# Kernel tuning notes

Hardware: AMD Instinct MI355X
Metric: run time of the kernel (lower is better)

The kernel has to match this reference:

```python
import jax, jax.numpy as jnp
import numpy as np

B, S, E = 2, 2048, 1024
H = 16
DH = E // H
FF = 4096
LN_EPS = 1e-5


def setup_inputs() -> dict:
    key = jax.random.key(0)
    ks = jax.random.split(key, 8)
    s_in = 1.0 / np.sqrt(E)
    s_ff = 1.0 / np.sqrt(FF)
    return {
        "x": jax.random.normal(ks[0], (B, S, E), dtype=jnp.float32),
        "w_qkv": jax.random.normal(ks[1], (E, 3 * E), dtype=jnp.float32) * s_in,
        "b_qkv": jnp.zeros((3 * E,), dtype=jnp.float32),
        "w_proj": jax.random.normal(ks[2], (E, E), dtype=jnp.float32) * s_in,
        "b_proj": jnp.zeros((E,), dtype=jnp.float32),
        "ln_g": jnp.ones((E,), dtype=jnp.float32),
        "ln_b": jnp.zeros((E,), dtype=jnp.float32),
        "w1": jax.random.normal(ks[3], (E, FF), dtype=jnp.float32) * s_in,
        "b1": jnp.zeros((FF,), dtype=jnp.float32),
        "w2": jax.random.normal(ks[4], (FF, E), dtype=jnp.float32) * s_ff,
        "b2": jnp.zeros((E,), dtype=jnp.float32),
    }


def reference(x, w_qkv, b_qkv, w_proj, b_proj, ln_g, ln_b, w1, b1, w2, b2):
    b, s, e = x.shape
    scale = e ** 0.5  # NOTE: original scales by sqrt(embed_dim), not sqrt(head_dim)
    # qkv projection then raw view to [B,3,H,S,Dh] (faithful to torch .view)
    qkv = (x @ w_qkv + b_qkv).reshape(b, 3, H, s, DH)
    q, k, v = qkv[:, 0], qkv[:, 1], qkv[:, 2]  # each [B,H,S,Dh]
    scores = jnp.einsum("bhqd,bhkd->bhqk", q, k) / scale  # [B,H,S,S]
    causal = jnp.tril(jnp.ones((s, s), dtype=bool))
    scores = jnp.where(causal, scores, -jnp.inf)
    attn = jax.nn.softmax(scores, axis=-1)
    h = jnp.einsum("bhqk,bhkd->bhqd", attn, v)  # [B,H,S,Dh]
    h = h.reshape(b, s, e)  # faithful raw view back to [B,S,E]
    h = h @ w_proj + b_proj  # dropout = identity (eval)
    # add & norm
    h = h + x
    mu = jnp.mean(h, axis=-1, keepdims=True)
    var = jnp.var(h, axis=-1, keepdims=True)
    h = (h - mu) * jax.lax.rsqrt(var + LN_EPS) * ln_g + ln_b
    # FFN (dropouts = identity in eval)
    out = jax.nn.relu(h @ w1 + b1) @ w2 + b2
    return out
```

## Files before the change

### kernel.cpp

```cpp
#include <hip/hip_runtime.h>

#define B_ 2
#define S_ 2048
#define E_ 1024
#define H_ 16
#define DH_ 64
#define FF_ 4096

typedef unsigned short bf16_t;
typedef __attribute__((ext_vector_type(8))) short bfrag;
typedef __attribute__((ext_vector_type(4))) float f32x4;
typedef __attribute__((ext_vector_type(16))) float f32x16;
typedef __attribute__((ext_vector_type(4))) unsigned int u32x4;

__device__ __forceinline__ bf16_t f2bf(float x) {
  union { float f; unsigned u; } c; c.f = x;
  return (bf16_t)((c.u + 0x7fffu + ((c.u >> 16) & 1u)) >> 16);
}

__device__ __forceinline__ unsigned pkbf(float lo, float hi) {
  unsigned r;
  asm("v_cvt_pk_bf16_f32 %0, %1, %2" : "=v"(r) : "v"(lo), "v"(hi));
  return r;
}

__device__ __forceinline__ void gload16(const void* g, void* l) {
  __builtin_amdgcn_global_load_lds(
      (const __attribute__((address_space(1))) void*)g,
      (__attribute__((address_space(3))) void*)l, 16, 0, 0);
}

__global__ __launch_bounds__(256) void cvt_kernel(const float* __restrict__ s,
                                                  bf16_t* __restrict__ d) {
  const int i = blockIdx.x * 256 + threadIdx.x;
  const float4 v = ((const float4*)s)[i];
  union { bf16_t u[4]; uint2 uv; } o;
  o.u[0] = f2bf(v.x); o.u[1] = f2bf(v.y); o.u[2] = f2bf(v.z); o.u[3] = f2bf(v.w);
  *(uint2*)(d + (size_t)i * 4) = o.uv;
}

__global__ void transpose_cvt(const float* __restrict__ src, bf16_t* __restrict__ dst,
                              int R, int C) {
  __shared__ float tile[32][33];
  const int c0 = blockIdx.x * 32, r0 = blockIdx.y * 32;
  const int tx = threadIdx.x, ty = threadIdx.y;
#pragma unroll
  for (int i = 0; i < 32; i += 8)
    tile[ty + i][tx] = src[(size_t)(r0 + ty + i) * C + c0 + tx];
  __syncthreads();
#pragma unroll
  for (int i = 0; i < 32; i += 8)
    dst[(size_t)(c0 + ty + i) * R + r0 + tx] = f2bf(tile[tx][ty + i]);
}

__global__ void vtrans_kernel(const bf16_t* __restrict__ qkv, bf16_t* __restrict__ vt) {
  const int bh = blockIdx.z;
  const int b = bh >> 4, h = bh & 15;
  const bf16_t* src = qkv + (size_t)b * S_ * 3 * E_ + (size_t)2 * H_ * S_ * DH_ +
                      (size_t)h * S_ * DH_;
  bf16_t* dst = vt + (size_t)bh * DH_ * S_;
  const int s0 = blockIdx.x * 32, d0 = blockIdx.y * 32;
  __shared__ bf16_t tile[32][33];
  const int tx = threadIdx.x, ty = threadIdx.y;
#pragma unroll
  for (int i = 0; i < 32; i += 8)
    tile[ty + i][tx] = src[(size_t)(s0 + ty + i) * DH_ + d0 + tx];
  __syncthreads();
#pragma unroll
  for (int i = 0; i < 32; i += 8)
    dst[(size_t)(d0 + ty + i) * S_ + s0 + tx] = tile[tx][ty + i];
}


__device__ __forceinline__ void stage_half(const bf16_t* __restrict__ G, int row0,
                                           int kbyte, int Kbytes, bf16_t* ldsreg,
                                           int w, int l) {
#pragma unroll
  for (int j = 0; j < 2; ++j) {
    const int chunk = j * 8 + w;
    const int r = chunk * 8 + (l >> 3);
    const int slot = ((l & 7) ^ (r & 7)) << 4;
    const char* src = (const char*)G + (size_t)(row0 + r) * Kbytes + kbyte + slot;
    gload16(src, (char*)ldsreg + chunk * 1024);
  }
}

__device__ __forceinline__ bfrag ldfrag(const bf16_t* __restrict__ reg, int r, int ks,
                                        int l) {
  int cb = ks * 64 + ((l >> 4) << 4);
  cb ^= (r & 7) << 4;
  return *(const bfrag*)((const char*)reg + r * 128 + cb);
}

template <int MODE>
__global__ __launch_bounds__(512, 2) void gemm8(
    const bf16_t* __restrict__ A, const bf16_t* __restrict__ Bt,
    const float* __restrict__ bias, const float* __restrict__ resid,
    float* __restrict__ outF, bf16_t* __restrict__ outB,
    int M, int N, int K, int ktiles) {
  __shared__ __align__(16) bf16_t lds4[4][256 * 64];
  const int tid = threadIdx.x;
  const int w = tid >> 6, l = tid & 63;
  const int wr = (w >> 2) * 128, wc = (w & 3) * 64;
  const int m0t = blockIdx.y * 256, n0t = blockIdx.x * 256;
  const int Kb = K * 2;
  const int kt0 = (MODE == 4) ? (int)blockIdx.z * ktiles : 0;
  const int ktEnd = kt0 + ktiles;
  if (MODE == 4) outF += (size_t)blockIdx.z * (size_t)M * N;

  stage_half(A, m0t, kt0 * 128, Kb, lds4[0], w, l);
  stage_half(A, m0t + 128, kt0 * 128, Kb, lds4[0] + 8192, w, l);
  stage_half(Bt, n0t, kt0 * 128, Kb, lds4[1], w, l);
  stage_half(Bt, n0t + 128, kt0 * 128, Kb, lds4[1] + 8192, w, l);
  stage_half(Bt, n0t, (kt0 + 1) * 128, Kb, lds4[3], w, l);
  stage_half(Bt, n0t + 128, (kt0 + 1) * 128, Kb, lds4[3] + 8192, w, l);
  asm volatile("s_waitcnt vmcnt(4)" ::: "memory");
  __builtin_amdgcn_s_barrier();

  f32x4 acc[8][4] = {};
  const int fr = l & 15;

  for (int t2 = kt0; t2 < ktEnd; t2 += 2) {
#pragma unroll
    for (int d = 0; d < 2; ++d) {
      const bf16_t* Ar = lds4[d * 2];
      const bf16_t* Br = lds4[d * 2 + 1];
      int sa = t2 + 1 + d; if (sa >= ktEnd) sa = kt0;
      int sb = t2 + 2 + d; if (sb >= ktEnd) sb = kt0;
      bfrag bfr[4][2], afr[2][2];
#pragma unroll
      for (int p = 0; p < 4; ++p) {
        if (p == 0) {
#pragma unroll
          for (int n = 0; n < 4; ++n)
#pragma unroll
            for (int ks = 0; ks < 2; ++ks)
              bfr[n][ks] = ldfrag(Br, wc + n * 16 + fr, ks, l);
        }
#pragma unroll
        for (int mm = 0; mm < 2; ++mm)
#pragma unroll
          for (int ks = 0; ks < 2; ++ks)
            afr[mm][ks] = ldfrag(Ar, wr + p * 32 + mm * 16 + fr, ks, l);
        if (p == 0)      stage_half(A, m0t, sa * 128, Kb, lds4[(d ^ 1) * 2], w, l);
        else if (p == 1) stage_half(A, m0t + 128, sa * 128, Kb, lds4[(d ^ 1) * 2] + 8192, w, l);
        else if (p == 2) stage_half(Bt, n0t, sb * 128, Kb, lds4[d * 2 + 1], w, l);
        else             stage_half(Bt, n0t + 128, sb * 128, Kb, lds4[d * 2 + 1] + 8192, w, l);
        __builtin_amdgcn_s_barrier();
        asm volatile("s_waitcnt lgkmcnt(0)" ::: "memory");
        __builtin_amdgcn_sched_barrier(0);
        __builtin_amdgcn_s_setprio(1);
#pragma unroll
        for (int mm = 0; mm < 2; ++mm)
#pragma unroll
          for (int n = 0; n < 4; ++n)
#pragma unroll
            for (int ks = 0; ks < 2; ++ks)
              acc[p * 2 + mm][n] = __builtin_amdgcn_mfma_f32_16x16x32_bf16(
                  afr[mm][ks], bfr[n][ks], acc[p * 2 + mm][n], 0, 0, 0);
        __builtin_amdgcn_s_setprio(0);
        if (p == 3) asm volatile("s_waitcnt vmcnt(4)" ::: "memory");
        __builtin_amdgcn_s_barrier();
      }
    }
  }

  const int cr = (l >> 4) * 4, cc = l & 15;
#pragma unroll
  for (int n = 0; n < 4; ++n) {
    const int gc = n0t + wc + n * 16 + cc;
    const float bn = (MODE == 4) ? 0.f : bias[gc];
#pragma unroll
    for (int m = 0; m < 8; ++m) {
      const int gr0 = m0t + wr + m * 16 + cr;
#pragma unroll
      for (int j = 0; j < 4; ++j) {
        float v = acc[m][n][j] + bn;
        const size_t idx = (size_t)(gr0 + j) * N + gc;
        if (MODE == 1) v += resid[idx];
        if (MODE == 2) v = fmaxf(v, 0.f);
        if (MODE == 0 || MODE == 2) outB[idx] = f2bf(v);
        else outF[idx] = v;
      }
    }
  }
}

__global__ __launch_bounds__(256) void red4_kernel(const float* __restrict__ p,
                                                   const float* __restrict__ bias,
                                                   float* __restrict__ out) {
  const size_t i = ((size_t)blockIdx.x * 256 + threadIdx.x) * 4;
  const size_t PS = (size_t)4096 * 1024;
  const float4 a = *(const float4*)(p + i);
  const float4 b = *(const float4*)(p + PS + i);
  const float4 c = *(const float4*)(p + 2 * PS + i);
  const float4 d = *(const float4*)(p + 3 * PS + i);
  const float4 bb = *(const float4*)(bias + (i & 1023));
  float4 o;
  o.x = a.x + b.x + c.x + d.x + bb.x;
  o.y = a.y + b.y + c.y + d.y + bb.y;
  o.z = a.z + b.z + c.z + d.z + bb.z;
  o.w = a.w + b.w + c.w + d.w + bb.w;
  *(float4*)(out + i) = o;
}

#define C1_ 0.0450842213f

template <bool MASK>
__device__ __forceinline__ void attn_step(const bf16_t* __restrict__ Kp,
                                          const bf16_t* __restrict__ Vt,
                                          int kv0, const bfrag* qf, f32x16& o0,
                                          f32x16& o1, float& m, float& lsum,
                                          int lq32, int hi) {
  bfrag kf[4];
#pragma unroll
  for (int c = 0; c < 4; ++c)
    kf[c] = *(const bfrag*)&Kp[(size_t)(kv0 + lq32) * DH_ + c * 16 + hi * 8];
  f32x16 st;
#pragma unroll
  for (int j = 0; j < 16; ++j) st[j] = 0.f;
#pragma unroll
  for (int c = 0; c < 4; ++c)
    st = __builtin_amdgcn_mfma_f32_32x32x16_bf16(kf[c], qf[c], st, 0, 0, 0);
  if (MASK) {
#pragma unroll
    for (int r = 0; r < 16; ++r) {
      const int kvloc = (r & 3) + 8 * (r >> 2) + 4 * hi;
      st[r] = (kvloc <= lq32) ? st[r] : -3.0e38f;
    }
  }
  float pm = st[0];
#pragma unroll
  for (int j = 1; j < 16; ++j) pm = fmaxf(pm, st[j]);
  pm = fmaxf(pm, __shfl_xor(pm, 32));
  if (!__all(pm <= m + 128.0f)) {
    const float mn = fmaxf(m, pm);
    const float corr = exp2f((m - mn) * C1_);
    m = mn;
    lsum *= corr;
#pragma unroll
    for (int j = 0; j < 16; ++j) { o0[j] *= corr; o1[j] *= corr; }
  }
  const float mc = m * C1_;
  float p[16];
  float ps = 0.f;
#pragma unroll
  for (int j = 0; j < 16; ++j) {
    p[j] = exp2f(__builtin_fmaf(st[j], C1_, -mc));
    ps += p[j];
  }
  ps += __shfl_xor(ps, 32);
  lsum += ps;
  unsigned wv[8], ov[8];
#pragma unroll
  for (int j = 0; j < 8; ++j) wv[j] = pkbf(p[2 * j], p[2 * j + 1]);
#pragma unroll
  for (int j = 0; j < 8; ++j) ov[j] = (unsigned)__shfl_xor((int)wv[j], 32);
  union { unsigned u[4]; bfrag f; } f0, f1;
  f0.u[0] = hi ? ov[2] : wv[0];
  f0.u[1] = hi ? ov[3] : wv[1];
  f0.u[2] = hi ? wv[2] : ov[0];
  f0.u[3] = hi ? wv[3] : ov[1];
  f1.u[0] = hi ? ov[6] : wv[4];
  f1.u[1] = hi ? ov[7] : wv[5];
  f1.u[2] = hi ? wv[6] : ov[4];
  f1.u[3] = hi ? wv[7] : ov[5];
#pragma unroll
  for (int t = 0; t < 2; ++t) {
    const bf16_t* vr = &Vt[(size_t)(t * 32 + lq32) * S_ + kv0 + hi * 8];
    bfrag v0 = *(const bfrag*)vr;
    bfrag v1 = *(const bfrag*)(vr + 16);
    f32x16& ot = t ? o1 : o0;
    ot = __builtin_amdgcn_mfma_f32_32x32x16_bf16(v0, f0.f, ot, 0, 0, 0);
    ot = __builtin_amdgcn_mfma_f32_32x32x16_bf16(v1, f1.f, ot, 0, 0, 0);
  }
}

__global__ __launch_bounds__(256, 3) void attn_kernel(const bf16_t* __restrict__ qkv,
                                                      const bf16_t* __restrict__ vt,
                                                      bf16_t* __restrict__ outp) {
  __shared__ unsigned short ot[4][32 * 72];
  const int tid = threadIdx.x;
  const int w = tid >> 6, l = tid & 63;
  const int lq32 = l & 31, hi = l >> 5;
  const int by = blockIdx.y;
  const int b = by >> 4, h = by & 15;
  const int qt = (by & 16) ? (15 - (int)blockIdx.x) : (int)blockIdx.x;
  const size_t bbase = (size_t)b * S_ * 3 * E_;
  const bf16_t* Q = qkv + bbase + (size_t)h * S_ * DH_;
  const bf16_t* Kp = Q + (size_t)H_ * S_ * DH_;
  const bf16_t* Vt = vt + (size_t)by * DH_ * S_;
  bf16_t* Og = outp + (size_t)by * S_ * DH_;
  const int q0w = qt * 128 + w * 32;

  bfrag qf[4];
#pragma unroll
  for (int c = 0; c < 4; ++c)
    qf[c] = *(const bfrag*)&Q[(size_t)(q0w + lq32) * DH_ + c * 16 + hi * 8];

  f32x16 o0, o1;
#pragma unroll
  for (int j = 0; j < 16; ++j) { o0[j] = 0.f; o1[j] = 0.f; }
  float m = -3.0e38f, lsum = 0.f;

  const int nfull = q0w >> 5;
  for (int s = 0; s < nfull; ++s)
    attn_step<false>(Kp, Vt, s * 32, qf, o0, o1, m, lsum, lq32, hi);
  attn_step<true>(Kp, Vt, q0w, qf, o0, o1, m, lsum, lq32, hi);

  const float linv = 1.0f / lsum;
  unsigned short* otw = ot[w];
#pragma unroll
  for (int t = 0; t < 2; ++t) {
    const f32x16& oo = t ? o1 : o0;
#pragma unroll
    for (int g = 0; g < 4; ++g) {
      const int d = t * 32 + g * 8 + hi * 4;
      uint2 v;
      v.x = pkbf(oo[g * 4 + 0] * linv, oo[g * 4 + 1] * linv);
      v.y = pkbf(oo[g * 4 + 2] * linv, oo[g * 4 + 3] * linv);
      *(uint2*)&otw[lq32 * 72 + d] = v;
    }
  }
  asm volatile("s_waitcnt lgkmcnt(0)" ::: "memory");
  const int q = l >> 1, hh = l & 1;
#pragma unroll
  for (int i = 0; i < 4; ++i) {
    u32x4 v = *(const u32x4*)&otw[q * 72 + hh * 32 + i * 8];
    *(u32x4*)&Og[(size_t)(q0w + q) * DH_ + hh * 32 + i * 8] = v;
  }
}

__global__ __launch_bounds__(256) void ln_kernel(const float* __restrict__ hin,
                                                 const float* __restrict__ g,
                                                 const float* __restrict__ be,
                                                 bf16_t* __restrict__ outp) {
  const int row = blockIdx.x;
  const int t = threadIdx.x;
  const float4 v = ((const float4*)(hin + (size_t)row * E_))[t];
  float s = v.x + v.y + v.z + v.w;
  float q = v.x * v.x + v.y * v.y + v.z * v.z + v.w * v.w;
#pragma unroll
  for (int d = 1; d < 64; d <<= 1) { s += __shfl_xor(s, d); q += __shfl_xor(q, d); }
  __shared__ float red[8];
  const int w = t >> 6;
  if ((t & 63) == 0) { red[w] = s; red[4 + w] = q; }
  __syncthreads();
  s = red[0] + red[1] + red[2] + red[3];
  q = red[4] + red[5] + red[6] + red[7];
  const float mu = s * (1.f / E_);
  const float var = q * (1.f / E_) - mu * mu;
  const float rs = rsqrtf(var + 1e-5f);
  const float4 gg = ((const float4*)g)[t];
  const float4 bb = ((const float4*)be)[t];
  union { bf16_t u[4]; uint2 uv; } o;
  o.u[0] = f2bf((v.x - mu) * rs * gg.x + bb.x);
  o.u[1] = f2bf((v.y - mu) * rs * gg.y + bb.y);
  o.u[2] = f2bf((v.z - mu) * rs * gg.z + bb.z);
  o.u[3] = f2bf((v.w - mu) * rs * gg.w + bb.w);
  *(uint2*)(outp + (size_t)row * E_ + t * 4) = o.uv;
}

extern "C" void kernel_launch(void* const* d_in, const int* in_sizes, int n_in,
                              void* d_out, int out_size, void* d_ws, size_t ws_size,
                              hipStream_t stream) {
  (void)in_sizes; (void)n_in; (void)out_size;
  const float* x      = (const float*)d_in[0];
  const float* w_qkv  = (const float*)d_in[1];
  const float* b_qkv  = (const float*)d_in[2];
  const float* w_proj = (const float*)d_in[3];
  const float* b_proj = (const float*)d_in[4];
  const float* ln_g   = (const float*)d_in[5];
  const float* ln_b   = (const float*)d_in[6];
  const float* w1     = (const float*)d_in[7];
  const float* b1     = (const float*)d_in[8];
  const float* w2     = (const float*)d_in[9];
  const float* b2     = (const float*)d_in[10];
  float* out = (float*)d_out;
  char* ws = (char*)d_ws;
  const size_t MB = (size_t)1 << 20;
  bf16_t* w2T    = (bf16_t*)(ws + 0 * MB);
  bf16_t* w1T    = (bf16_t*)(ws + 8 * MB);
  bf16_t* ffn1b  = (bf16_t*)(ws + 16 * MB);
  bf16_t* vtb    = (bf16_t*)(ws + 16 * MB);
  bf16_t* wqkvT  = (bf16_t*)(ws + 24 * MB);
  bf16_t* wprojT = (bf16_t*)(ws + 30 * MB);
  bf16_t* attnb  = (bf16_t*)(ws + 32 * MB);
  bf16_t* xb     = (bf16_t*)(ws + 40 * MB);
  float*  parts  = (float*)(ws + 48 * MB);
  bf16_t* qkvb   = (bf16_t*)(ws + 48 * MB);
  bf16_t* lnb    = (bf16_t*)(ws + 48 * MB);
  float*  hbuf   = (float*)(ws + 72 * MB);
  const bool splitk = ws_size >= 112 * MB;

  dim3 tb(32, 8);
  cvt_kernel<<<4096, 256, 0, stream>>>(x, xb);
  transpose_cvt<<<dim3(3072 / 32, 1024 / 32), tb, 0, stream>>>(w_qkv, wqkvT, 1024, 3072);
  transpose_cvt<<<dim3(1024 / 32, 1024 / 32), tb, 0, stream>>>(w_proj, wprojT, 1024, 1024);
  transpose_cvt<<<dim3(4096 / 32, 1024 / 32), tb, 0, stream>>>(w1, w1T, 1024, 4096);
  transpose_cvt<<<dim3(1024 / 32, 4096 / 32), tb, 0, stream>>>(w2, w2T, 4096, 1024);

  gemm8<0><<<dim3(12, 16), 512, 0, stream>>>(xb, wqkvT, b_qkv, nullptr, nullptr, qkvb,
                                             4096, 3072, 1024, 16);

  vtrans_kernel<<<dim3(S_ / 32, 2, 32), tb, 0, stream>>>(qkvb, vtb);
  attn_kernel<<<dim3(16, 32), 256, 0, stream>>>(qkvb, vtb, attnb);

  gemm8<1><<<dim3(4, 16), 512, 0, stream>>>(attnb, wprojT, b_proj, x, hbuf, nullptr,
                                            4096, 1024, 1024, 16);

  ln_kernel<<<4096, 256, 0, stream>>>(hbuf, ln_g, ln_b, lnb);

  gemm8<2><<<dim3(16, 16), 512, 0, stream>>>(lnb, w1T, b1, nullptr, nullptr, ffn1b,
                                             4096, 4096, 1024, 16);

  if (splitk) {
    gemm8<4><<<dim3(4, 16, 4), 512, 0, stream>>>(ffn1b, w2T, nullptr, nullptr, parts,
                                                 nullptr, 4096, 1024, 4096, 16);
    red4_kernel<<<4096, 256, 0, stream>>>(parts, b2, out);
  } else {
    gemm8<3><<<dim3(4, 16), 512, 0, stream>>>(ffn1b, w2T, b2, nullptr, out, nullptr,
                                              4096, 1024, 4096, 64);
  }
}
```

Before: 270.2 us.

## Split attention KV across warps, split-K proj GEMM with fused LN, halve FFN2 split

Attention now gives each block one 32-row query tile and spreads the KV steps across its four warps, merging the partial softmax states through shared memory. This raises the block count and balances the causal work better, at the cost of extra syncs and a cross-warp reduction. The output projection moves to a 2-way split-K GEMM whose partials are summed inside a new LayerNorm kernel together with bias and residual. The FFN2 split-K drops from 4 to 2 partitions, which cuts reduction traffic but leaves fewer blocks, and the workspace layout is reshuffled to fit.

```diff
diff --git a/kernel.cpp b/kernel.cpp
--- a/kernel.cpp
+++ b/kernel.cpp
@@ -186,21 +186,19 @@
   }
 }
 
-__global__ __launch_bounds__(256) void red4_kernel(const float* __restrict__ p,
+__global__ __launch_bounds__(256) void red2_kernel(const float* __restrict__ p,
                                                    const float* __restrict__ bias,
                                                    float* __restrict__ out) {
   const size_t i = ((size_t)blockIdx.x * 256 + threadIdx.x) * 4;
   const size_t PS = (size_t)4096 * 1024;
   const float4 a = *(const float4*)(p + i);
   const float4 b = *(const float4*)(p + PS + i);
-  const float4 c = *(const float4*)(p + 2 * PS + i);
-  const float4 d = *(const float4*)(p + 3 * PS + i);
   const float4 bb = *(const float4*)(bias + (i & 1023));
   float4 o;
-  o.x = a.x + b.x + c.x + d.x + bb.x;
-  o.y = a.y + b.y + c.y + d.y + bb.y;
-  o.z = a.z + b.z + c.z + d.z + bb.z;
-  o.w = a.w + b.w + c.w + d.w + bb.w;
+  o.x = a.x + b.x + bb.x;
+  o.y = a.y + b.y + bb.y;
+  o.z = a.z + b.z + bb.z;
+  o.w = a.w + b.w + bb.w;
   *(float4*)(out + i) = o;
 }
 
@@ -276,68 +274,98 @@
   }
 }
 
-__global__ __launch_bounds__(256, 3) void attn_kernel(const bf16_t* __restrict__ qkv,
+__global__ __launch_bounds__(256, 6) void attn_kernel(const bf16_t* __restrict__ qkv,
                                                       const bf16_t* __restrict__ vt,
                                                       bf16_t* __restrict__ outp) {
-  __shared__ unsigned short ot[4][32 * 72];
+  __shared__ float obuf[2][32][66];
+  __shared__ float ml[4][2][32];
+  __shared__ float lst[32];
   const int tid = threadIdx.x;
   const int w = tid >> 6, l = tid & 63;
   const int lq32 = l & 31, hi = l >> 5;
   const int by = blockIdx.y;
   const int b = by >> 4, h = by & 15;
-  const int qt = (by & 16) ? (15 - (int)blockIdx.x) : (int)blockIdx.x;
+  const int qblk = (by & 16) ? (63 - (int)blockIdx.x) : (int)blockIdx.x;
   const size_t bbase = (size_t)b * S_ * 3 * E_;
   const bf16_t* Q = qkv + bbase + (size_t)h * S_ * DH_;
   const bf16_t* Kp = Q + (size_t)H_ * S_ * DH_;
   const bf16_t* Vt = vt + (size_t)by * DH_ * S_;
   bf16_t* Og = outp + (size_t)by * S_ * DH_;
-  const int q0w = qt * 128 + w * 32;
+  const int q0 = qblk * 32;
 
   bfrag qf[4];
 #pragma unroll
   for (int c = 0; c < 4; ++c)
-    qf[c] = *(const bfrag*)&Q[(size_t)(q0w + lq32) * DH_ + c * 16 + hi * 8];
+    qf[c] = *(const bfrag*)&Q[(size_t)(q0 + lq32) * DH_ + c * 16 + hi * 8];
 
   f32x16 o0, o1;
 #pragma unroll
   for (int j = 0; j < 16; ++j) { o0[j] = 0.f; o1[j] = 0.f; }
   float m = -3.0e38f, lsum = 0.f;
 
-  const int nfull = q0w >> 5;
-  for (int s = 0; s < nfull; ++s)
+  const int nfull = qblk;
+  for (int s = w; s < nfull; s += 4)
     attn_step<false>(Kp, Vt, s * 32, qf, o0, o1, m, lsum, lq32, hi);
-  attn_step<true>(Kp, Vt, q0w, qf, o0, o1, m, lsum, lq32, hi);
-
-  const float linv = 1.0f / lsum;
-  unsigned short* otw = ot[w];
-#pragma unroll
-  for (int t = 0; t < 2; ++t) {
-    const f32x16& oo = t ? o1 : o0;
-#pragma unroll
-    for (int g = 0; g < 4; ++g) {
-      const int d = t * 32 + g * 8 + hi * 4;
-      uint2 v;
-      v.x = pkbf(oo[g * 4 + 0] * linv, oo[g * 4 + 1] * linv);
-      v.y = pkbf(oo[g * 4 + 2] * linv, oo[g * 4 + 3] * linv);
-      *(uint2*)&otw[lq32 * 72 + d] = v;
+  if ((nfull & 3) == w)
+    attn_step<true>(Kp, Vt, q0, qf, o0, o1, m, lsum, lq32, hi);
+
+  if (hi == 0) { ml[w][0][lq32] = m; ml[w][1][lq32] = lsum; }
+  __syncthreads();
+  const float m0 = ml[0][0][lq32], m1 = ml[1][0][lq32];
+  const float m2 = ml[2][0][lq32], m3 = ml[3][0][lq32];
+  const float mstar = fmaxf(fmaxf(m0, m1), fmaxf(m2, m3));
+  const float lstar = ml[0][1][lq32] * exp2f((m0 - mstar) * C1_) +
+                      ml[1][1][lq32] * exp2f((m1 - mstar) * C1_) +
+                      ml[2][1][lq32] * exp2f((m2 - mstar) * C1_) +
+                      ml[3][1][lq32] * exp2f((m3 - mstar) * C1_);
+  if (w == 0 && hi == 0) lst[lq32] = lstar;
+  const float myscale = exp2f((m - mstar) * C1_);
+#pragma unroll
+  for (int j = 0; j < 16; ++j) { o0[j] *= myscale; o1[j] *= myscale; }
+  if (w < 2) {
+#pragma unroll
+    for (int t = 0; t < 2; ++t) {
+      const f32x16& oo = t ? o1 : o0;
+#pragma unroll
+      for (int g = 0; g < 4; ++g) {
+        const int d = t * 32 + g * 8 + hi * 4;
+        *(float2*)&obuf[w][lq32][d] = make_float2(oo[g * 4 + 0], oo[g * 4 + 1]);
+        *(float2*)&obuf[w][lq32][d + 2] = make_float2(oo[g * 4 + 2], oo[g * 4 + 3]);
+      }
     }
   }
-  asm volatile("s_waitcnt lgkmcnt(0)" ::: "memory");
-  const int q = l >> 1, hh = l & 1;
-#pragma unroll
-  for (int i = 0; i < 4; ++i) {
-    u32x4 v = *(const u32x4*)&otw[q * 72 + hh * 32 + i * 8];
-    *(u32x4*)&Og[(size_t)(q0w + q) * DH_ + hh * 32 + i * 8] = v;
-  }
-}
-
-__global__ __launch_bounds__(256) void ln_kernel(const float* __restrict__ hin,
-                                                 const float* __restrict__ g,
-                                                 const float* __restrict__ be,
-                                                 bf16_t* __restrict__ outp) {
-  const int row = blockIdx.x;
-  const int t = threadIdx.x;
-  const float4 v = ((const float4*)(hin + (size_t)row * E_))[t];
+  __syncthreads();
+  if (w >= 2) {
+#pragma unroll
+    for (int t = 0; t < 2; ++t) {
+      const f32x16& oo = t ? o1 : o0;
+#pragma unroll
+      for (int g = 0; g < 4; ++g) {
+        const int d = t * 32 + g * 8 + hi * 4;
+        float2 a = *(const float2*)&obuf[w - 2][lq32][d];
+        float2 c = *(const float2*)&obuf[w - 2][lq32][d + 2];
+        a.x += oo[g * 4 + 0]; a.y += oo[g * 4 + 1];
+        c.x += oo[g * 4 + 2]; c.y += oo[g * 4 + 3];
+        *(float2*)&obuf[w - 2][lq32][d] = a;
+        *(float2*)&obuf[w - 2][lq32][d + 2] = c;
+      }
+    }
+  }
+  __syncthreads();
+  const int q = tid >> 3, dc = (tid & 7) * 8;
+  const float linv = 1.0f / lst[q];
+  union { unsigned u[4]; u32x4 v; } pk;
+#pragma unroll
+  for (int g = 0; g < 4; ++g) {
+    float2 a = *(const float2*)&obuf[0][q][dc + g * 2];
+    float2 c = *(const float2*)&obuf[1][q][dc + g * 2];
+    pk.u[g] = pkbf((a.x + c.x) * linv, (a.y + c.y) * linv);
+  }
+  *(u32x4*)&Og[(size_t)(q0 + q) * DH_ + dc] = pk.v;
+}
+
+__device__ __forceinline__ void ln_core(float4 v, int t, const float* g,
+                                        const float* be, bf16_t* orow) {
   float s = v.x + v.y + v.z + v.w;
   float q = v.x * v.x + v.y * v.y + v.z * v.z + v.w * v.w;
 #pragma unroll
@@ -358,7 +386,37 @@
   o.u[1] = f2bf((v.y - mu) * rs * gg.y + bb.y);
   o.u[2] = f2bf((v.z - mu) * rs * gg.z + bb.z);
   o.u[3] = f2bf((v.w - mu) * rs * gg.w + bb.w);
-  *(uint2*)(outp + (size_t)row * E_ + t * 4) = o.uv;
+  *(uint2*)(orow + t * 4) = o.uv;
+}
+
+__global__ __launch_bounds__(256) void ln_kernel(const float* __restrict__ hin,
+                                                 const float* __restrict__ g,
+                                                 const float* __restrict__ be,
+                                                 bf16_t* __restrict__ outp) {
+  const int row = blockIdx.x, t = threadIdx.x;
+  const float4 v = ((const float4*)(hin + (size_t)row * E_))[t];
+  ln_core(v, t, g, be, outp + (size_t)row * E_);
+}
+
+__global__ __launch_bounds__(256) void ln2_kernel(const float* __restrict__ p,
+                                                  const float* __restrict__ x,
+                                                  const float* __restrict__ bproj,
+                                                  const float* __restrict__ g,
+                                                  const float* __restrict__ be,
+                                                  bf16_t* __restrict__ outp) {
+  const int row = blockIdx.x, t = threadIdx.x;
+  const size_t PS = (size_t)4096 * 1024;
+  const size_t off = (size_t)row * E_ + t * 4;
+  const float4 a = *(const float4*)(p + off);
+  const float4 b = *(const float4*)(p + PS + off);
+  const float4 xr = *(const float4*)(x + off);
+  const float4 bp = *(const float4*)(bproj + t * 4);
+  float4 v;
+  v.x = a.x + b.x + xr.x + bp.x;
+  v.y = a.y + b.y + xr.y + bp.y;
+  v.z = a.z + b.z + xr.z + bp.z;
+  v.w = a.w + b.w + xr.w + bp.w;
+  ln_core(v, t, g, be, outp + (size_t)row * E_);
 }
 
 extern "C" void kernel_launch(void* const* d_in, const int* in_sizes, int n_in,
@@ -381,16 +439,17 @@
   const size_t MB = (size_t)1 << 20;
   bf16_t* w2T    = (bf16_t*)(ws + 0 * MB);
   bf16_t* w1T    = (bf16_t*)(ws + 8 * MB);
-  bf16_t* ffn1b  = (bf16_t*)(ws + 16 * MB);
   bf16_t* vtb    = (bf16_t*)(ws + 16 * MB);
+  bf16_t* lnb    = (bf16_t*)(ws + 16 * MB);
   bf16_t* wqkvT  = (bf16_t*)(ws + 24 * MB);
   bf16_t* wprojT = (bf16_t*)(ws + 30 * MB);
   bf16_t* attnb  = (bf16_t*)(ws + 32 * MB);
   bf16_t* xb     = (bf16_t*)(ws + 40 * MB);
-  float*  parts  = (float*)(ws + 48 * MB);
   bf16_t* qkvb   = (bf16_t*)(ws + 48 * MB);
-  bf16_t* lnb    = (bf16_t*)(ws + 48 * MB);
-  float*  hbuf   = (float*)(ws + 72 * MB);
+  float*  pparts = (float*)(ws + 48 * MB);
+  float*  hbuf   = (float*)(ws + 48 * MB);
+  bf16_t* ffn1b  = (bf16_t*)(ws + 48 * MB);
+  float*  fparts = (float*)(ws + 80 * MB);
   const bool splitk = ws_size >= 112 * MB;
 
   dim3 tb(32, 8);
@@ -404,21 +463,23 @@
                                              4096, 3072, 1024, 16);
 
   vtrans_kernel<<<dim3(S_ / 32, 2, 32), tb, 0, stream>>>(qkvb, vtb);
-  attn_kernel<<<dim3(16, 32), 256, 0, stream>>>(qkvb, vtb, attnb);
-
-  gemm8<1><<<dim3(4, 16), 512, 0, stream>>>(attnb, wprojT, b_proj, x, hbuf, nullptr,
-                                            4096, 1024, 1024, 16);
-
-  ln_kernel<<<4096, 256, 0, stream>>>(hbuf, ln_g, ln_b, lnb);
-
-  gemm8<2><<<dim3(16, 16), 512, 0, stream>>>(lnb, w1T, b1, nullptr, nullptr, ffn1b,
-                                             4096, 4096, 1024, 16);
+  attn_kernel<<<dim3(64, 32), 256, 0, stream>>>(qkvb, vtb, attnb);
 
   if (splitk) {
-    gemm8<4><<<dim3(4, 16, 4), 512, 0, stream>>>(ffn1b, w2T, nullptr, nullptr, parts,
-                                                 nullptr, 4096, 1024, 4096, 16);
-    red4_kernel<<<4096, 256, 0, stream>>>(parts, b2, out);
+    gemm8<4><<<dim3(4, 16, 2), 512, 0, stream>>>(attnb, wprojT, nullptr, nullptr,
+                                                 pparts, nullptr, 4096, 1024, 1024, 8);
+    ln2_kernel<<<4096, 256, 0, stream>>>(pparts, x, b_proj, ln_g, ln_b, lnb);
+    gemm8<2><<<dim3(16, 16), 512, 0, stream>>>(lnb, w1T, b1, nullptr, nullptr, ffn1b,
+                                               4096, 4096, 1024, 16);
+    gemm8<4><<<dim3(4, 16, 2), 512, 0, stream>>>(ffn1b, w2T, nullptr, nullptr, fparts,
+                                                 nullptr, 4096, 1024, 4096, 32);
+    red2_kernel<<<4096, 256, 0, stream>>>(fparts, b2, out);
   } else {
+    gemm8<1><<<dim3(4, 16), 512, 0, stream>>>(attnb, wprojT, b_proj, x, hbuf, nullptr,
+                                              4096, 1024, 1024, 16);
+    ln_kernel<<<4096, 256, 0, stream>>>(hbuf, ln_g, ln_b, lnb);
+    gemm8<2><<<dim3(16, 16), 512, 0, stream>>>(lnb, w1T, b1, nullptr, nullptr, ffn1b,
+                                               4096, 4096, 1024, 16);
     gemm8<3><<<dim3(4, 16), 512, 0, stream>>>(ffn1b, w2T, b2, nullptr, out, nullptr,
                                               4096, 1024, 4096, 64);
   }
```

After: 326.5 us. 20.8% more time.
